# Optimization experiments

Measured on AMD Instinct MI355X. Metric: run time of the kernel, lower is better.

## Reference

```python
import jax, jax.numpy as jnp
import numpy as np

B, C, H, T, L = 128, 16, 9, 2048, 9  # batch, channels, sensors, time, decomp levels
TAU = 1.0

def _conv(x, w, pad):
    # x: [N,C,H,W], w: [O,I,kh,kw]
    return jax.lax.conv_general_dilated(x, w, (1, 1), pad,
                                        dimension_numbers=('NCHW', 'OIHW', 'NCHW'))

def _prelu(x, a):
    return jnp.where(x >= 0, x, a * x)

def _branch(z, w1, a, w2):
    # ReflectionPad2d((1,1,0,0)) -> Conv(1,3) -> PReLU -> Conv(1,1) -> Tanh
    z = jnp.pad(z, ((0, 0), (0, 0), (0, 0), (1, 1)), mode='reflect')
    z = _prelu(_conv(z, w1, [(0, 0), (0, 0)]), a)
    return jnp.tanh(_conv(z, w2, [(0, 0), (0, 0)]))


def setup_inputs() -> dict:
    key = jax.random.key(0)
    ks = jax.random.split(key, 24)
    n = lambda k, s, sc=0.05: jax.random.normal(k, s, dtype=jnp.float32) * sc
    u = jax.random.uniform(ks[1], (L, 2 * B, 2, 1, 1), dtype=jnp.float32,
                           minval=1e-6, maxval=1.0 - 1e-6)
    inp = {
        'x': jax.random.normal(ks[0], (B, 1, H, T), dtype=jnp.float32),
        'gumbel_noise': -jnp.log(-jnp.log(u)),
        # conv_in stem
        'Wc1': n(ks[2], (C, 1, 1, 33)), 'bc1': jnp.zeros((C,), jnp.float32),
        'bn1_g': jnp.ones((C,), jnp.float32), 'bn1_b': jnp.zeros((C,), jnp.float32),
        'a_c1': jnp.float32(0.25),
        'Wc2': n(ks[3], (C, C, 1, 3)), 'bc2': jnp.zeros((C,), jnp.float32),
        'bn2_g': jnp.ones((C,), jnp.float32), 'bn2_b': jnp.zeros((C,), jnp.float32),
        'a_c2': jnp.float32(0.25),
        # per-level lifting P/U branches
        'WP1': n(ks[4], (L, C, C, 1, 3)), 'aP': jnp.full((L,), 0.25, jnp.float32),
        'WP2': n(ks[5], (L, C, C, 1, 1)),
        'WU1': n(ks[6], (L, C, C, 1, 3)), 'aU': jnp.full((L,), 0.25, jnp.float32),
        'WU2': n(ks[7], (L, C, C, 1, 1)),
        # per-level gumble routing head (pooled -> 1x1 C->C -> PReLU -> 1x1 C->2 -> PReLU)
        'Wg1': n(ks[8], (L, C, C, 1, 1)), 'ag1': jnp.full((L,), 0.25, jnp.float32),
        'Wg2': n(ks[9], (L, 2, C, 1, 1)), 'ag2': jnp.full((L,), 0.25, jnp.float32),
    }
    return inp


def _forward(x, Wc1, bc1, bn1_g, bn1_b, a_c1, Wc2, bc2, bn2_g, bn2_b, a_c2,
             WP1, aP, WP2, WU1, aU, WU2, Wg1, ag1, Wg2, ag2, gumbel_noise):
    rs = lambda v: v.reshape(1, -1, 1, 1)
    # conv_in stem (BatchNorm in eval form with default running stats)
    x = _conv(x, Wc1, [(0, 0), (16, 16)]) + rs(bc1)
    x = _prelu(x * rs(bn1_g) + rs(bn1_b), a_c1)
    x = _conv(x, Wc2, [(0, 0), (1, 1)]) + rs(bc2)
    x = _prelu(x * rs(bn2_g) + rs(bn2_b), a_c2)  # [B,C,H,T]

    feats = []
    for i in range(L):
        even, odd = x[..., ::2], x[..., 1::2]
        # modified lifting: c = even + U(odd); d = odd - P(c)
        c = even + _branch(odd, WU1[i], aU[i], WU2[i])
        d = odd - _branch(c, WP1[i], aP[i], WP2[i])
        out = jnp.stack([c, d], axis=1)  # [B,2,C,H,t]
        t = out.shape[-1]
        # gumble_block_2D: pool each (low/high) slice to [2B,C,1,1]
        pooled = out.reshape(B * 2, C, H, t).mean(axis=(2, 3), keepdims=True)
        hm = _prelu(_conv(pooled, Wg1[i], [(0, 0), (0, 0)]), ag1[i])
        hm = _prelu(_conv(hm, Wg2[i], [(0, 0), (0, 0)]), ag2[i])  # [2B,2,1,1]
        s = jax.nn.softmax(hm, axis=1)
        m = jax.nn.softmax((s + gumbel_noise[i]) / TAU, axis=1)
        m = m.reshape(B, 2, 2, 1, 1)
        input_conv = out * m[:, :, 0][..., None]  # gated conv branch [B,2,C,H,t]
        input_res = out * m[:, :, 1][..., None]   # gated residual branch
        feats.append(input_res.mean(axis=-1))      # [B,2,C,H]
        x = input_conv[:, 0]                       # gated low-pass feeds next level
    return jnp.stack(feats, axis=-1)  # [B,2,C,H,L]


def reference(x, gumbel_noise, Wc1, bc1, bn1_g, bn1_b, a_c1, Wc2, bc2, bn2_g,
              bn2_b, a_c2, WP1, aP, WP2, WU1, aU, WU2, Wg1, ag1, Wg2, ag2):
    return _forward(x, Wc1, bc1, bn1_g, bn1_b, a_c1, Wc2, bc2, bn2_g, bn2_b,
                    a_c2, WP1, aP, WP2, WU1, aU, WU2, Wg1, ag1, Wg2, ag2,
                    gumbel_noise)
```

## Files before the change

### kernel.cpp

```cpp
#include <hip/hip_runtime.h>
#include <hip/hip_bf16.h>


#define CB 16
#define HH 9
#define TT0 2048
#define RS_SLOT 36864
#define LPITCH 20

__device__ __forceinline__ float ftanh(float x) {
    float e = __expf(2.f * x);
    return 1.f - 2.f / (e + 1.f);
}
__device__ __forceinline__ float fprelu(float v, float a) {
    return v >= 0.f ? v : a * v;
}
__device__ __forceinline__ void ld16(const float* p, float* v) {
#pragma unroll
    for (int q = 0; q < 4; ++q) {
        float4 f = *(const float4*)(p + 4 * q);
        v[4 * q] = f.x; v[4 * q + 1] = f.y; v[4 * q + 2] = f.z; v[4 * q + 3] = f.w;
    }
}
__device__ __forceinline__ void st16(float* p, const float* v) {
#pragma unroll
    for (int q = 0; q < 4; ++q) {
        float4 f; f.x = v[4 * q]; f.y = v[4 * q + 1]; f.z = v[4 * q + 2]; f.w = v[4 * q + 3];
        *(float4*)(p + 4 * q) = f;
    }
}

__device__ __forceinline__ void rowsum_reduce(const float* vals, float* rs, int tile,
                                              int b, int h, int sdx, int tid) {
    __shared__ float red[4 * CB];
    const int lane = tid & 63, wv = tid >> 6;
#pragma unroll
    for (int cc = 0; cc < CB; ++cc) {
        float s = vals[cc];
#pragma unroll
        for (int off = 32; off >= 1; off >>= 1) s += __shfl_xor(s, off, 64);
        if (lane == cc) red[wv * CB + cc] = s;
    }
    __syncthreads();
    if (tid < CB) {
        float s = red[tid] + red[CB + tid] + red[2 * CB + tid] + red[3 * CB + tid];
        rs[(size_t)tile * RS_SLOT + ((size_t)(2 * b + sdx) * CB + tid) * HH + h] = s;
    }
}

__global__ void wtrans_kernel(const float* __restrict__ Wc1, const float* __restrict__ Wc2,
                              const float* __restrict__ WU1, const float* __restrict__ WU2,
                              const float* __restrict__ WP1, const float* __restrict__ WP2,
                              float* __restrict__ W)
{
    const int tid = threadIdx.x;
    for (int idx = tid; idx < 528; idx += 256) {
        int k = idx >> 4, cc = idx & 15;
        W[idx] = Wc1[cc * 33 + k];
    }
    for (int idx = tid; idx < 768; idx += 256) {
        int k = idx >> 8, c2 = (idx >> 4) & 15, cc = idx & 15;
        W[528 + idx] = Wc2[(cc * 16 + c2) * 3 + k];
    }
    for (int i = 0; i < 9; ++i) {
        float* base = W + 1296 + i * 2048;
        const float* wu1 = WU1 + i * 768;
        const float* wp1 = WP1 + i * 768;
        const float* wu2 = WU2 + i * 256;
        const float* wp2 = WP2 + i * 256;
        for (int idx = tid; idx < 768; idx += 256) {
            int k = idx >> 8, c2 = (idx >> 4) & 15, cc = idx & 15;
            base[idx]        = wu1[cc * 48 + c2 * 3 + k];
            base[1024 + idx] = wp1[cc * 48 + c2 * 3 + k];
        }
        if (tid < 256) {
            int idx = tid;
            if (idx < 256) {
                int c2 = idx >> 4, cc = idx & 15;
                base[768 + idx]  = wu2[cc * 16 + c2];
                base[1792 + idx] = wp2[cc * 16 + c2];
            }
        }
    }
}

__global__ __launch_bounds__(256, 4) void front_kernel(
    const float* __restrict__ x, const float* __restrict__ Wt,
    const float* __restrict__ bc1,
    const float* __restrict__ bn1g, const float* __restrict__ bn1b,
    const float* __restrict__ ac1,
    const float* __restrict__ bc2,
    const float* __restrict__ bn2g, const float* __restrict__ bn2b,
    const float* __restrict__ ac2,
    float* __restrict__ y)
{
    const int tid = threadIdx.x;
    const int t0  = blockIdx.x * 254;
    const int h   = blockIdx.y;
    const int b   = blockIdx.z;
    const float* Wc1t = Wt;
    const float* Wc2t = Wt + 528;

    __shared__ float lds_x[288];
    __shared__ float lds_y[256 * LPITCH];

    const float* xrow = x + (size_t)(b * HH + h) * TT0;
    {
        int g = t0 - 17 + tid;
        lds_x[tid] = (g >= 0 && g < TT0) ? xrow[g] : 0.f;
        if (tid < 32) {
            int g2 = t0 + 239 + tid;
            lds_x[256 + tid] = (g2 >= 0 && g2 < TT0) ? xrow[g2] : 0.f;
        }
    }
    __syncthreads();

    const float a1 = ac1[0], a2 = ac2[0];
    float acc[CB];
#pragma unroll
    for (int cc = 0; cc < CB; ++cc) acc[cc] = bc1[cc];
#pragma unroll
    for (int k = 0; k < 33; ++k) {
        float xv = lds_x[tid + k];
        const float* wp = Wc1t + k * 16;
#pragma unroll
        for (int cc = 0; cc < CB; ++cc) acc[cc] = fmaf(wp[cc], xv, acc[cc]);
    }
#pragma unroll
    for (int cc = 0; cc < CB; ++cc)
        lds_y[tid * LPITCH + cc] = fprelu(acc[cc] * bn1g[cc] + bn1b[cc], a1);
    __syncthreads();

    const int jt = t0 + tid;
    if (tid < 254 && jt < TT0) {
        float acc2[CB];
#pragma unroll
        for (int cc = 0; cc < CB; ++cc) acc2[cc] = bc2[cc];
#pragma unroll
        for (int k = 0; k < 3; ++k) {
            int u = jt - 1 + k;
            if (u >= 0 && u < TT0) {
                float yv[CB];
                ld16(&lds_y[(tid + k) * LPITCH], yv);
#pragma unroll
                for (int c2 = 0; c2 < CB; ++c2) {
                    float yvv = yv[c2];
                    const float* wp = Wc2t + (k * 16 + c2) * 16;
#pragma unroll
                    for (int cc = 0; cc < CB; ++cc)
                        acc2[cc] = fmaf(wp[cc], yvv, acc2[cc]);
                }
            }
        }
        float ov[CB];
#pragma unroll
        for (int cc = 0; cc < CB; ++cc) ov[cc] = fprelu(acc2[cc] * bn2g[cc] + bn2b[cc], a2);
        st16(y + ((size_t)(b * HH + h) * TT0 + jt) * CB, ov);
    }
}

__global__ __launch_bounds__(256, 2) void c_kernel(
    const float* __restrict__ xin, float* __restrict__ xout,
    float* __restrict__ rs, const float* __restrict__ m0prev,
    const float* __restrict__ Wt,
    const float* __restrict__ aUp, const int t)
{
    const int tid  = threadIdx.x;
    const int row  = blockIdx.x;
    const int tile = blockIdx.y;
    const int b = row / 9, h = row - 9 * b;
    const float sm = m0prev ? m0prev[b] : 1.f;
    const float aU = aUp[0];
    const float* xrow = xin + (size_t)row * (2 * t) * CB;
    const int p0 = tile * 1024;
    const float* WU1t = Wt;
    const float* WU2t = Wt + 768;

    float accz[4][CB];
#pragma unroll
    for (int g = 0; g < 4; ++g)
#pragma unroll
        for (int i = 0; i < CB; ++i) accz[g][i] = 0.f;

#pragma unroll
    for (int k = 0; k < 3; ++k) {
#pragma unroll
        for (int g = 0; g < 4; ++g) {
            const int j = p0 + g * 256 + tid;
            if (j < t) {
                int u = j - 1 + k;
                int um = u < 0 ? -u : (u >= t ? 2 * t - 2 - u : u);
                float ow[CB];
                ld16(xrow + (size_t)(2 * um + 1) * CB, ow);
#pragma unroll
                for (int c2 = 0; c2 < CB; ++c2) {
                    float o = ow[c2];
                    const float* wp = WU1t + (k * 16 + c2) * 16;
#pragma unroll
                    for (int cc = 0; cc < CB; ++cc)
                        accz[g][cc] = fmaf(wp[cc], o, accz[g][cc]);
                }
            }
        }
    }

    float sc[CB];
#pragma unroll
    for (int i = 0; i < CB; ++i) sc[i] = 0.f;

#pragma unroll
    for (int g = 0; g < 4; ++g) {
        const int j = p0 + g * 256 + tid;
        if (j < t) {
            float az[CB];
#pragma unroll
            for (int i = 0; i < CB; ++i) az[i] = fprelu(accz[g][i], aU);
            float bacc[CB];
#pragma unroll
            for (int cc = 0; cc < CB; ++cc) bacc[cc] = 0.f;
#pragma unroll
            for (int c2 = 0; c2 < CB; ++c2) {
                float z = az[c2];
                const float* wp = WU2t + c2 * 16;
#pragma unroll
                for (int cc = 0; cc < CB; ++cc)
                    bacc[cc] = fmaf(wp[cc], z, bacc[cc]);
            }
            float ev[CB];
            ld16(xrow + (size_t)(2 * j) * CB, ev);
            float cv[CB];
#pragma unroll
            for (int cc = 0; cc < CB; ++cc) {
                cv[cc] = sm * ev[cc] + ftanh(sm * bacc[cc]);
                sc[cc] += cv[cc];
            }
            st16(xout + ((size_t)row * t + j) * CB, cv);
        }
    }
    rowsum_reduce(sc, rs, tile, b, h, 0, tid);
}

__global__ __launch_bounds__(256, 2) void d_kernel(
    const float* __restrict__ xin, const float* __restrict__ cbuf,
    float* __restrict__ rs, const float* __restrict__ m0prev,
    const float* __restrict__ Wt,
    const float* __restrict__ aPp, const int t)
{
    const int tid  = threadIdx.x;
    const int row  = blockIdx.x;
    const int tile = blockIdx.y;
    const int b = row / 9, h = row - 9 * b;
    const float sm = m0prev ? m0prev[b] : 1.f;
    const float aP = aPp[0];
    const float* xrow = xin + (size_t)row * (2 * t) * CB;
    const float* crow = cbuf + (size_t)row * t * CB;
    const int p0 = tile * 1024;
    const float* WP1t = Wt;
    const float* WP2t = Wt + 768;

    float accz[4][CB];
#pragma unroll
    for (int g = 0; g < 4; ++g)
#pragma unroll
        for (int i = 0; i < CB; ++i) accz[g][i] = 0.f;

#pragma unroll
    for (int k = 0; k < 3; ++k) {
#pragma unroll
        for (int g = 0; g < 4; ++g) {
            const int j = p0 + g * 256 + tid;
            if (j < t) {
                int u = j - 1 + k;
                int um = u < 0 ? -u : (u >= t ? 2 * t - 2 - u : u);
                float cw[CB];
                ld16(crow + (size_t)um * CB, cw);
#pragma unroll
                for (int c2 = 0; c2 < CB; ++c2) {
                    float o = cw[c2];
                    const float* wp = WP1t + (k * 16 + c2) * 16;
#pragma unroll
                    for (int cc = 0; cc < CB; ++cc)
                        accz[g][cc] = fmaf(wp[cc], o, accz[g][cc]);
                }
            }
        }
    }

    float sd[CB];
#pragma unroll
    for (int i = 0; i < CB; ++i) sd[i] = 0.f;

#pragma unroll
    for (int g = 0; g < 4; ++g) {
        const int j = p0 + g * 256 + tid;
        if (j < t) {
            float az[CB];
#pragma unroll
            for (int i = 0; i < CB; ++i) az[i] = fprelu(accz[g][i], aP);
            float bacc[CB];
#pragma unroll
            for (int cc = 0; cc < CB; ++cc) bacc[cc] = 0.f;
#pragma unroll
            for (int c2 = 0; c2 < CB; ++c2) {
                float z = az[c2];
                const float* wp = WP2t + c2 * 16;
#pragma unroll
                for (int cc = 0; cc < CB; ++cc)
                    bacc[cc] = fmaf(wp[cc], z, bacc[cc]);
            }
            float ov[CB];
            ld16(xrow + (size_t)(2 * j + 1) * CB, ov);
#pragma unroll
            for (int cc = 0; cc < CB; ++cc)
                sd[cc] += sm * ov[cc] - ftanh(bacc[cc]);
        }
    }
    rowsum_reduce(sd, rs, tile, b, h, 1, tid);
}

__global__ __launch_bounds__(192) void gate_kernel(
    const float* __restrict__ rs, const float* __restrict__ gn,
    const float* __restrict__ Wg1, const float* __restrict__ ag1p,
    const float* __restrict__ Wg2, const float* __restrict__ ag2p,
    float* __restrict__ out, float* __restrict__ m0buf,
    const int t, const int nt, const int li)
{
    const int bj  = blockIdx.x;
    const int tid = threadIdx.x;

    __shared__ float sums[144];
    __shared__ float sscale;

    if (tid < 144) {
        float s = 0.f;
        for (int tl = 0; tl < nt; ++tl)
            s += rs[(size_t)tl * RS_SLOT + (size_t)bj * 144 + tid];
        sums[tid] = s;
    }
    __syncthreads();

    if (tid == 0) {
        const float ag1 = ag1p[0], ag2 = ag2p[0];
        const float inv = 1.f / (9.f * (float)t);
        float pooled[CB];
#pragma unroll
        for (int cc = 0; cc < CB; ++cc) {
            float s = 0.f;
#pragma unroll
            for (int h = 0; h < HH; ++h) s += sums[cc * HH + h];
            pooled[cc] = s * inv;
        }
        float hm1[CB];
#pragma unroll
        for (int cc = 0; cc < CB; ++cc) {
            float s = 0.f;
#pragma unroll
            for (int c2 = 0; c2 < CB; ++c2) s = fmaf(Wg1[cc * CB + c2], pooled[c2], s);
            hm1[cc] = fprelu(s, ag1);
        }
        float h0 = 0.f, h1 = 0.f;
#pragma unroll
        for (int c2 = 0; c2 < CB; ++c2) {
            h0 = fmaf(Wg2[c2], hm1[c2], h0);
            h1 = fmaf(Wg2[CB + c2], hm1[c2], h1);
        }
        h0 = fprelu(h0, ag2); h1 = fprelu(h1, ag2);
        float mx = fmaxf(h0, h1);
        float e0 = __expf(h0 - mx), e1 = __expf(h1 - mx);
        float s0 = e0 / (e0 + e1), s1 = e1 / (e0 + e1);
        float a0 = s0 + gn[bj * 2 + 0], a1 = s1 + gn[bj * 2 + 1];
        float mx2 = fmaxf(a0, a1);
        float f0 = __expf(a0 - mx2), f1 = __expf(a1 - mx2);
        float m0 = f0 / (f0 + f1), m1 = f1 / (f0 + f1);
        sscale = m1 / (float)t;
        if ((bj & 1) == 0) m0buf[bj >> 1] = m0;
    }
    __syncthreads();

    if (tid < 144)
        out[(size_t)(bj * 144 + tid) * 9 + li] = sums[tid] * sscale;
}

extern "C" void kernel_launch(void* const* d_in, const int* in_sizes, int n_in,
                              void* d_out, int out_size, void* d_ws, size_t ws_size,
                              hipStream_t stream) {
    const float* x    = (const float*)d_in[0];
    const float* gn   = (const float*)d_in[1];
    const float* Wc1  = (const float*)d_in[2];
    const float* bc1  = (const float*)d_in[3];
    const float* bn1g = (const float*)d_in[4];
    const float* bn1b = (const float*)d_in[5];
    const float* ac1  = (const float*)d_in[6];
    const float* Wc2  = (const float*)d_in[7];
    const float* bc2  = (const float*)d_in[8];
    const float* bn2g = (const float*)d_in[9];
    const float* bn2b = (const float*)d_in[10];
    const float* ac2  = (const float*)d_in[11];
    const float* WP1  = (const float*)d_in[12];
    const float* aP   = (const float*)d_in[13];
    const float* WP2  = (const float*)d_in[14];
    const float* WU1  = (const float*)d_in[15];
    const float* aU   = (const float*)d_in[16];
    const float* WU2  = (const float*)d_in[17];
    const float* Wg1  = (const float*)d_in[18];
    const float* ag1  = (const float*)d_in[19];
    const float* Wg2  = (const float*)d_in[20];
    const float* ag2  = (const float*)d_in[21];
    float* out = (float*)d_out;

    char* ws = (char*)d_ws;
    const size_t sz0 = (size_t)128 * 9 * 2048 * 16 * 4;
    const size_t sz1 = sz0 / 2;
    float* buf0 = (float*)ws;
    float* buf1 = (float*)(ws + sz0);
    float* rs   = (float*)(ws + sz0 + sz1);
    float* m0b  = (float*)(ws + sz0 + sz1 + (size_t)4 * RS_SLOT * 4);
    float* wt   = (float*)(ws + sz0 + sz1 + (size_t)4 * RS_SLOT * 4 + 512);

    wtrans_kernel<<<1, 256, 0, stream>>>(Wc1, Wc2, WU1, WU2, WP1, WP2, wt);

    dim3 fgrid(9, 9, 128);
    front_kernel<<<fgrid, 256, 0, stream>>>(x, wt, bc1, bn1g, bn1b, ac1,
                                            bc2, bn2g, bn2b, ac2, buf0);

    float* cur = buf0;
    float* nxt = buf1;
    int t = 1024;
    for (int i = 0; i < 9; ++i) {
        const int nt = (t + 1023) >> 10;
        const float* m0p = (i == 0) ? nullptr : m0b;
        const float* lw = wt + 1296 + i * 2048;
        dim3 lgrid(128 * 9, nt);
        c_kernel<<<lgrid, 256, 0, stream>>>(cur, nxt, rs, m0p, lw, aU + i, t);
        d_kernel<<<lgrid, 256, 0, stream>>>(cur, nxt, rs, m0p, lw + 1024, aP + i, t);
        gate_kernel<<<256, 192, 0, stream>>>(
            rs, gn + i * 512, Wg1 + i * 256, ag1 + i, Wg2 + i * 32, ag2 + i,
            out, m0b, t, nt, i);
        float* tmp = cur; cur = nxt; nxt = tmp;
        t >>= 1;
    }
}
```

Before: 792.4 us.

## Fuse lifting update/predict kernels and collapse final levels into one per-batch kernel

Merges the separate update (c) and predict (d) kernels into one kernel. The c values for a 256-wide tile plus two halo points are staged in shared memory, so the predict step no longer re-reads c from global memory. Tiles shrink from 1024 to 256 positions to get more blocks per row, and the odd sample is reused from the update pass. The last four small decomposition levels, including the gating math, now run in a single tail kernel per batch entirely in LDS. This removes many tiny launches, at the cost of recomputing halo points and using shared-memory atomics for the row sums.

Measured after the change: 1.080 ms. 36.2% more time.

```diff
diff --git a/kernel.cpp b/kernel.cpp
--- a/kernel.cpp
+++ b/kernel.cpp
@@ -22,18 +22,29 @@
         v[4 * q] = f.x; v[4 * q + 1] = f.y; v[4 * q + 2] = f.z; v[4 * q + 3] = f.w;
     }
 }
+__device__ __forceinline__ void ld16s(const float* p, float* v) {
+#pragma unroll
+    for (int q = 0; q < 4; ++q) {
+        float4 f = *(const float4*)(p + 4 * q);
+        v[4 * q] = f.x; v[4 * q + 1] = f.y; v[4 * q + 2] = f.z; v[4 * q + 3] = f.w;
+    }
+}
 __device__ __forceinline__ void st16(float* p, const float* v) {
 #pragma unroll
     for (int q = 0; q < 4; ++q) {
         float4 f; f.x = v[4 * q]; f.y = v[4 * q + 1]; f.z = v[4 * q + 2]; f.w = v[4 * q + 3];
         *(float4*)(p + 4 * q) = f;
     }
+}
+__device__ __forceinline__ int refl(int u, int t) {
+    return u < 0 ? -u : (u >= t ? 2 * t - 2 - u : u);
 }
 
 __device__ __forceinline__ void rowsum_reduce(const float* vals, float* rs, int tile,
                                               int b, int h, int sdx, int tid) {
     __shared__ float red[4 * CB];
     const int lane = tid & 63, wv = tid >> 6;
+    __syncthreads();
 #pragma unroll
     for (int cc = 0; cc < CB; ++cc) {
         float s = vals[cc];
@@ -73,7 +84,7 @@
             base[idx]        = wu1[cc * 48 + c2 * 3 + k];
             base[1024 + idx] = wp1[cc * 48 + c2 * 3 + k];
         }
-        if (tid < 256) {
+        {
             int idx = tid;
             if (idx < 256) {
                 int c2 = idx >> 4, cc = idx & 15;
@@ -82,6 +93,52 @@
             }
         }
     }
+}
+
+__device__ __forceinline__ void compute_c(
+    const float* __restrict__ xrow, int j, int t, float sm,
+    const float* __restrict__ W1, const float* __restrict__ W2, float aU,
+    float* cv, float* ow1)
+{
+    float accz[CB];
+#pragma unroll
+    for (int i = 0; i < CB; ++i) accz[i] = 0.f;
+#pragma unroll
+    for (int k = 0; k < 3; ++k) {
+        int um = refl(j - 1 + k, t);
+        float ow[CB];
+        ld16(xrow + (size_t)(2 * um + 1) * CB, ow);
+        if (k == 1) {
+#pragma unroll
+            for (int i = 0; i < CB; ++i) ow1[i] = ow[i];
+        }
+#pragma unroll
+        for (int c2 = 0; c2 < CB; ++c2) {
+            float o = ow[c2];
+            const float* wp = W1 + (k * 16 + c2) * 16;
+#pragma unroll
+            for (int cc = 0; cc < CB; ++cc)
+                accz[cc] = fmaf(wp[cc], o, accz[cc]);
+        }
+    }
+#pragma unroll
+    for (int i = 0; i < CB; ++i) accz[i] = fprelu(accz[i], aU);
+    float bacc[CB];
+#pragma unroll
+    for (int cc = 0; cc < CB; ++cc) bacc[cc] = 0.f;
+#pragma unroll
+    for (int c2 = 0; c2 < CB; ++c2) {
+        float z = accz[c2];
+        const float* wp = W2 + c2 * 16;
+#pragma unroll
+        for (int cc = 0; cc < CB; ++cc)
+            bacc[cc] = fmaf(wp[cc], z, bacc[cc]);
+    }
+    float ev[CB];
+    ld16(xrow + (size_t)(2 * j) * CB, ev);
+#pragma unroll
+    for (int cc = 0; cc < CB; ++cc)
+        cv[cc] = sm * ev[cc] + ftanh(sm * bacc[cc]);
 }
 
 __global__ __launch_bounds__(256, 4) void front_kernel(
@@ -141,7 +198,7 @@
             int u = jt - 1 + k;
             if (u >= 0 && u < TT0) {
                 float yv[CB];
-                ld16(&lds_y[(tid + k) * LPITCH], yv);
+                ld16s(&lds_y[(tid + k) * LPITCH], yv);
 #pragma unroll
                 for (int c2 = 0; c2 < CB; ++c2) {
                     float yvv = yv[c2];
@@ -159,163 +216,91 @@
     }
 }
 
-__global__ __launch_bounds__(256, 2) void c_kernel(
+__global__ __launch_bounds__(256, 2) void cd_kernel(
     const float* __restrict__ xin, float* __restrict__ xout,
     float* __restrict__ rs, const float* __restrict__ m0prev,
     const float* __restrict__ Wt,
-    const float* __restrict__ aUp, const int t)
+    const float* __restrict__ aUp, const float* __restrict__ aPp, const int t)
 {
     const int tid  = threadIdx.x;
     const int row  = blockIdx.x;
     const int tile = blockIdx.y;
     const int b = row / 9, h = row - 9 * b;
     const float sm = m0prev ? m0prev[b] : 1.f;
-    const float aU = aUp[0];
+    const float aU = aUp[0], aP = aPp[0];
     const float* xrow = xin + (size_t)row * (2 * t) * CB;
-    const int p0 = tile * 1024;
+    const int p0 = tile * 256;
+    const int j = p0 + tid;
+    const bool valid = (j < t);
+
     const float* WU1t = Wt;
     const float* WU2t = Wt + 768;
-
-    float accz[4][CB];
-#pragma unroll
-    for (int g = 0; g < 4; ++g)
-#pragma unroll
-        for (int i = 0; i < CB; ++i) accz[g][i] = 0.f;
-
-#pragma unroll
-    for (int k = 0; k < 3; ++k) {
-#pragma unroll
-        for (int g = 0; g < 4; ++g) {
-            const int j = p0 + g * 256 + tid;
-            if (j < t) {
-                int u = j - 1 + k;
-                int um = u < 0 ? -u : (u >= t ? 2 * t - 2 - u : u);
-                float ow[CB];
-                ld16(xrow + (size_t)(2 * um + 1) * CB, ow);
-#pragma unroll
-                for (int c2 = 0; c2 < CB; ++c2) {
-                    float o = ow[c2];
-                    const float* wp = WU1t + (k * 16 + c2) * 16;
-#pragma unroll
-                    for (int cc = 0; cc < CB; ++cc)
-                        accz[g][cc] = fmaf(wp[cc], o, accz[g][cc]);
-                }
-            }
-        }
-    }
-
-    float sc[CB];
-#pragma unroll
-    for (int i = 0; i < CB; ++i) sc[i] = 0.f;
-
-#pragma unroll
-    for (int g = 0; g < 4; ++g) {
-        const int j = p0 + g * 256 + tid;
-        if (j < t) {
-            float az[CB];
-#pragma unroll
-            for (int i = 0; i < CB; ++i) az[i] = fprelu(accz[g][i], aU);
-            float bacc[CB];
-#pragma unroll
-            for (int cc = 0; cc < CB; ++cc) bacc[cc] = 0.f;
+    const float* WP1t = Wt + 1024;
+    const float* WP2t = Wt + 1792;
+
+    __shared__ float ldc[258 * LPITCH];
+
+    float cv[CB], ow1[CB];
+#pragma unroll
+    for (int i = 0; i < CB; ++i) { cv[i] = 0.f; ow1[i] = 0.f; }
+
+    if (valid) {
+        compute_c(xrow, j, t, sm, WU1t, WU2t, aU, cv, ow1);
+        st16(&ldc[(tid + 1) * LPITCH], cv);
+        st16(xout + ((size_t)row * t + j) * CB, cv);
+    }
+    if (tid < 2) {
+        int jx = (tid == 0) ? p0 - 1 : p0 + 256;
+        if (jx >= 0 && jx < t) {
+            float hv[CB], dump[CB];
+            compute_c(xrow, jx, t, sm, WU1t, WU2t, aU, hv, dump);
+            st16(&ldc[(jx - p0 + 1) * LPITCH], hv);
+        }
+    }
+
+    rowsum_reduce(cv, rs, tile, b, h, 0, tid);
+
+    float dv[CB];
+#pragma unroll
+    for (int i = 0; i < CB; ++i) dv[i] = 0.f;
+
+    if (valid) {
+        float accz[CB];
+#pragma unroll
+        for (int i = 0; i < CB; ++i) accz[i] = 0.f;
+#pragma unroll
+        for (int k = 0; k < 3; ++k) {
+            int um = refl(j - 1 + k, t);
+            int li = um - p0 + 1;
+            float cw[CB];
+            ld16s(&ldc[li * LPITCH], cw);
 #pragma unroll
             for (int c2 = 0; c2 < CB; ++c2) {
-                float z = az[c2];
-                const float* wp = WU2t + c2 * 16;
+                float o = cw[c2];
+                const float* wp = WP1t + (k * 16 + c2) * 16;
 #pragma unroll
                 for (int cc = 0; cc < CB; ++cc)
-                    bacc[cc] = fmaf(wp[cc], z, bacc[cc]);
-            }
-            float ev[CB];
-            ld16(xrow + (size_t)(2 * j) * CB, ev);
-            float cv[CB];
-#pragma unroll
-            for (int cc = 0; cc < CB; ++cc) {
-                cv[cc] = sm * ev[cc] + ftanh(sm * bacc[cc]);
-                sc[cc] += cv[cc];
-            }
-            st16(xout + ((size_t)row * t + j) * CB, cv);
-        }
-    }
-    rowsum_reduce(sc, rs, tile, b, h, 0, tid);
-}
-
-__global__ __launch_bounds__(256, 2) void d_kernel(
-    const float* __restrict__ xin, const float* __restrict__ cbuf,
-    float* __restrict__ rs, const float* __restrict__ m0prev,
-    const float* __restrict__ Wt,
-    const float* __restrict__ aPp, const int t)
-{
-    const int tid  = threadIdx.x;
-    const int row  = blockIdx.x;
-    const int tile = blockIdx.y;
-    const int b = row / 9, h = row - 9 * b;
-    const float sm = m0prev ? m0prev[b] : 1.f;
-    const float aP = aPp[0];
-    const float* xrow = xin + (size_t)row * (2 * t) * CB;
-    const float* crow = cbuf + (size_t)row * t * CB;
-    const int p0 = tile * 1024;
-    const float* WP1t = Wt;
-    const float* WP2t = Wt + 768;
-
-    float accz[4][CB];
-#pragma unroll
-    for (int g = 0; g < 4; ++g)
-#pragma unroll
-        for (int i = 0; i < CB; ++i) accz[g][i] = 0.f;
-
-#pragma unroll
-    for (int k = 0; k < 3; ++k) {
-#pragma unroll
-        for (int g = 0; g < 4; ++g) {
-            const int j = p0 + g * 256 + tid;
-            if (j < t) {
-                int u = j - 1 + k;
-                int um = u < 0 ? -u : (u >= t ? 2 * t - 2 - u : u);
-                float cw[CB];
-                ld16(crow + (size_t)um * CB, cw);
-#pragma unroll
-                for (int c2 = 0; c2 < CB; ++c2) {
-                    float o = cw[c2];
-                    const float* wp = WP1t + (k * 16 + c2) * 16;
-#pragma unroll
-                    for (int cc = 0; cc < CB; ++cc)
-                        accz[g][cc] = fmaf(wp[cc], o, accz[g][cc]);
-                }
-            }
-        }
-    }
-
-    float sd[CB];
-#pragma unroll
-    for (int i = 0; i < CB; ++i) sd[i] = 0.f;
-
-#pragma unroll
-    for (int g = 0; g < 4; ++g) {
-        const int j = p0 + g * 256 + tid;
-        if (j < t) {
-            float az[CB];
-#pragma unroll
-            for (int i = 0; i < CB; ++i) az[i] = fprelu(accz[g][i], aP);
-            float bacc[CB];
-#pragma unroll
-            for (int cc = 0; cc < CB; ++cc) bacc[cc] = 0.f;
-#pragma unroll
-            for (int c2 = 0; c2 < CB; ++c2) {
-                float z = az[c2];
-                const float* wp = WP2t + c2 * 16;
-#pragma unroll
-                for (int cc = 0; cc < CB; ++cc)
-                    bacc[cc] = fmaf(wp[cc], z, bacc[cc]);
-            }
-            float ov[CB];
-            ld16(xrow + (size_t)(2 * j + 1) * CB, ov);
+                    accz[cc] = fmaf(wp[cc], o, accz[cc]);
+            }
+        }
+#pragma unroll
+        for (int i = 0; i < CB; ++i) accz[i] = fprelu(accz[i], aP);
+        float bacc[CB];
+#pragma unroll
+        for (int cc = 0; cc < CB; ++cc) bacc[cc] = 0.f;
+#pragma unroll
+        for (int c2 = 0; c2 < CB; ++c2) {
+            float z = accz[c2];
+            const float* wp = WP2t + c2 * 16;
 #pragma unroll
             for (int cc = 0; cc < CB; ++cc)
-                sd[cc] += sm * ov[cc] - ftanh(bacc[cc]);
-        }
-    }
-    rowsum_reduce(sd, rs, tile, b, h, 1, tid);
+                bacc[cc] = fmaf(wp[cc], z, bacc[cc]);
+        }
+#pragma unroll
+        for (int cc = 0; cc < CB; ++cc)
+            dv[cc] = sm * ow1[cc] - ftanh(bacc[cc]);
+    }
+    rowsum_reduce(dv, rs, tile, b, h, 1, tid);
 }
 
 __global__ __launch_bounds__(192) void gate_kernel(
@@ -379,6 +364,187 @@
 
     if (tid < 144)
         out[(size_t)(bj * 144 + tid) * 9 + li] = sums[tid] * sscale;
+}
+
+__global__ __launch_bounds__(256) void tail_kernel(
+    const float* __restrict__ xin,
+    const float* __restrict__ m0in,
+    const float* __restrict__ Wt,
+    const float* __restrict__ aUa, const float* __restrict__ aPa,
+    const float* __restrict__ gn,
+    const float* __restrict__ Wg1a, const float* __restrict__ ag1a,
+    const float* __restrict__ Wg2a, const float* __restrict__ ag2a,
+    float* __restrict__ out)
+{
+    const int b   = blockIdx.x;
+    const int tid = threadIdx.x;
+
+    __shared__ float bufA[9216];
+    __shared__ float bufB[4608];
+    __shared__ float sums[288];
+    __shared__ float sh_sm, sh_sc0, sh_sc1;
+
+    for (int idx = tid; idx < 9216; idx += 256)
+        bufA[idx] = xin[(size_t)b * 9216 + idx];
+    if (tid == 0) sh_sm = m0in[b];
+    __syncthreads();
+
+    float* cur = bufA;
+    float* cb  = bufB;
+    int t = 32;
+    for (int l = 5; l <= 8; ++l) {
+        const float* W    = Wt + 1296 + l * 2048;
+        const float* WU1t = W;
+        const float* WU2t = W + 768;
+        const float* WP1t = W + 1024;
+        const float* WP2t = W + 1792;
+        const float aU = aUa[l], aP = aPa[l];
+        const float sm = sh_sm;
+        const int t2 = 2 * t;
+
+        for (int idx = tid; idx < 288; idx += 256) sums[idx] = 0.f;
+        __syncthreads();
+
+        for (int item = tid; item < 9 * t; item += 256) {
+            int h = item / t, j = item - h * t;
+            const float* xr = cur + h * t2 * CB;
+            float accz[CB];
+#pragma unroll
+            for (int i = 0; i < CB; ++i) accz[i] = 0.f;
+#pragma unroll
+            for (int k = 0; k < 3; ++k) {
+                int um = refl(j - 1 + k, t);
+                float ow[CB];
+                ld16s(xr + (2 * um + 1) * CB, ow);
+#pragma unroll
+                for (int c2 = 0; c2 < CB; ++c2) {
+                    float o = ow[c2];
+                    const float* wp = WU1t + (k * 16 + c2) * 16;
+#pragma unroll
+                    for (int cc = 0; cc < CB; ++cc)
+                        accz[cc] = fmaf(wp[cc], o, accz[cc]);
+                }
+            }
+#pragma unroll
+            for (int i = 0; i < CB; ++i) accz[i] = fprelu(accz[i], aU);
+            float bacc[CB];
+#pragma unroll
+            for (int cc = 0; cc < CB; ++cc) bacc[cc] = 0.f;
+#pragma unroll
+            for (int c2 = 0; c2 < CB; ++c2) {
+                float z = accz[c2];
+                const float* wp = WU2t + c2 * 16;
+#pragma unroll
+                for (int cc = 0; cc < CB; ++cc)
+                    bacc[cc] = fmaf(wp[cc], z, bacc[cc]);
+            }
+            float ev[CB];
+            ld16s(xr + (2 * j) * CB, ev);
+            float cvv[CB];
+#pragma unroll
+            for (int cc = 0; cc < CB; ++cc) {
+                cvv[cc] = sm * ev[cc] + ftanh(sm * bacc[cc]);
+                atomicAdd(&sums[cc * HH + h], cvv[cc]);
+            }
+            st16(cb + (h * t + j) * CB, cvv);
+        }
+        __syncthreads();
+
+        for (int item = tid; item < 9 * t; item += 256) {
+            int h = item / t, j = item - h * t;
+            const float* xr = cur + h * t2 * CB;
+            const float* cr = cb + h * t * CB;
+            float accz[CB];
+#pragma unroll
+            for (int i = 0; i < CB; ++i) accz[i] = 0.f;
+#pragma unroll
+            for (int k = 0; k < 3; ++k) {
+                int um = refl(j - 1 + k, t);
+                float cw[CB];
+                ld16s(cr + um * CB, cw);
+#pragma unroll
+                for (int c2 = 0; c2 < CB; ++c2) {
+                    float o = cw[c2];
+                    const float* wp = WP1t + (k * 16 + c2) * 16;
+#pragma unroll
+                    for (int cc = 0; cc < CB; ++cc)
+                        accz[cc] = fmaf(wp[cc], o, accz[cc]);
+                }
+            }
+#pragma unroll
+            for (int i = 0; i < CB; ++i) accz[i] = fprelu(accz[i], aP);
+            float bacc[CB];
+#pragma unroll
+            for (int cc = 0; cc < CB; ++cc) bacc[cc] = 0.f;
+#pragma unroll
+            for (int c2 = 0; c2 < CB; ++c2) {
+                float z = accz[c2];
+                const float* wp = WP2t + c2 * 16;
+#pragma unroll
+                for (int cc = 0; cc < CB; ++cc)
+                    bacc[cc] = fmaf(wp[cc], z, bacc[cc]);
+            }
+            float ov[CB];
+            ld16s(xr + (2 * j + 1) * CB, ov);
+#pragma unroll
+            for (int cc = 0; cc < CB; ++cc)
+                atomicAdd(&sums[144 + cc * HH + h], sm * ov[cc] - ftanh(bacc[cc]));
+        }
+        __syncthreads();
+
+        if (tid < 2) {
+            const int s = tid;
+            const float ag1 = ag1a[l], ag2 = ag2a[l];
+            const float* Wg1 = Wg1a + l * 256;
+            const float* Wg2 = Wg2a + l * 32;
+            const float inv = 1.f / (9.f * (float)t);
+            float pooled[CB];
+#pragma unroll
+            for (int cc = 0; cc < CB; ++cc) {
+                float ss = 0.f;
+#pragma unroll
+                for (int h = 0; h < HH; ++h) ss += sums[s * 144 + cc * HH + h];
+                pooled[cc] = ss * inv;
+            }
+            float hm1[CB];
+#pragma unroll
+            for (int cc = 0; cc < CB; ++cc) {
+                float ss = 0.f;
+#pragma unroll
+                for (int c2 = 0; c2 < CB; ++c2) ss = fmaf(Wg1[cc * CB + c2], pooled[c2], ss);
+                hm1[cc] = fprelu(ss, ag1);
+            }
+            float h0 = 0.f, h1 = 0.f;
+#pragma unroll
+            for (int c2 = 0; c2 < CB; ++c2) {
+                h0 = fmaf(Wg2[c2], hm1[c2], h0);
+                h1 = fmaf(Wg2[CB + c2], hm1[c2], h1);
+            }
+            h0 = fprelu(h0, ag2); h1 = fprelu(h1, ag2);
+            float mx = fmaxf(h0, h1);
+            float e0 = __expf(h0 - mx), e1 = __expf(h1 - mx);
+            float s0 = e0 / (e0 + e1), s1 = e1 / (e0 + e1);
+            const int bj = b * 2 + s;
+            float a0 = s0 + gn[(size_t)l * 512 + bj * 2 + 0];
+            float a1 = s1 + gn[(size_t)l * 512 + bj * 2 + 1];
+            float mx2 = fmaxf(a0, a1);
+            float f0 = __expf(a0 - mx2), f1 = __expf(a1 - mx2);
+            float m0 = f0 / (f0 + f1), m1 = f1 / (f0 + f1);
+            if (s == 0) { sh_sc0 = m1 / (float)t; sh_sm = m0; }
+            else        { sh_sc1 = m1 / (float)t; }
+        }
+        __syncthreads();
+
+        for (int idx = tid; idx < 288; idx += 256) {
+            int s = idx / 144, rem = idx - s * 144;
+            float sc = s ? sh_sc1 : sh_sc0;
+            out[(size_t)(((b * 2 + s) * 144) + rem) * 9 + l] = sums[idx] * sc;
+        }
+        __syncthreads();
+
+        float* tmp = cur; cur = cb; cb = tmp;
+        t >>= 1;
+    }
 }
 
 extern "C" void kernel_launch(void* const* d_in, const int* in_sizes, int n_in,
@@ -426,17 +592,18 @@
     float* cur = buf0;
     float* nxt = buf1;
     int t = 1024;
-    for (int i = 0; i < 9; ++i) {
-        const int nt = (t + 1023) >> 10;
+    for (int i = 0; i < 5; ++i) {
+        const int nt = (t + 255) >> 8;
         const float* m0p = (i == 0) ? nullptr : m0b;
         const float* lw = wt + 1296 + i * 2048;
         dim3 lgrid(128 * 9, nt);
-        c_kernel<<<lgrid, 256, 0, stream>>>(cur, nxt, rs, m0p, lw, aU + i, t);
-        d_kernel<<<lgrid, 256, 0, stream>>>(cur, nxt, rs, m0p, lw + 1024, aP + i, t);
+        cd_kernel<<<lgrid, 256, 0, stream>>>(cur, nxt, rs, m0p, lw, aU + i, aP + i, t);
         gate_kernel<<<256, 192, 0, stream>>>(
             rs, gn + i * 512, Wg1 + i * 256, ag1 + i, Wg2 + i * 32, ag2 + i,
             out, m0b, t, nt, i);
         float* tmp = cur; cur = nxt; nxt = tmp;
         t >>= 1;
     }
-}
+    tail_kernel<<<128, 256, 0, stream>>>(cur, m0b, wt, aU, aP, gn,
+                                         Wg1, ag1, Wg2, ag2, out);
+}
```
